# Kernel tuning notes

Hardware: AMD Instinct MI355X
Metric: run time of the kernel (lower is better)

The kernel has to match this reference:

```python
import jax, jax.numpy as jnp
import numpy as np

D = 128
N_ITERS = 3
TAU = 0.5
SCALE = D ** -0.5
NF, NV, NA = 50000, 1024, 64


def _gelu(x):
    return jax.nn.gelu(x, approximate=False)  # torch nn.GELU default = exact erf


def setup_inputs() -> dict:
    key = jax.random.key(0)
    ks = jax.random.split(key, 16)
    s = 0.02
    return {
        "fact_embs": jax.random.normal(ks[0], (NF, D), jnp.float32),
        "var_init": jax.random.normal(ks[1], (NV, D), jnp.float32),
        "cooc_mask": jax.random.randint(ks[2], (NA, NV), 0, 2, jnp.int32),
        "gumbel_u": jax.random.uniform(ks[3], (NV, NF), jnp.float32, 1e-6, 1.0 - 1e-6),
        "Wq": jax.random.normal(ks[4], (D, D), jnp.float32) * s, "bq": jnp.zeros((D,), jnp.float32),
        "Wk": jax.random.normal(ks[5], (D, D), jnp.float32) * s, "bk": jnp.zeros((D,), jnp.float32),
        "Wv": jax.random.normal(ks[6], (D, D), jnp.float32) * s, "bv": jnp.zeros((D,), jnp.float32),
        "Wm1": jax.random.normal(ks[7], (2 * D, D), jnp.float32) * s, "bm1": jnp.zeros((D,), jnp.float32),
        "Wm2": jax.random.normal(ks[8], (D, D), jnp.float32) * s, "bm2": jnp.zeros((D,), jnp.float32),
        "Wc1": jax.random.normal(ks[9], (2 * D, D), jnp.float32) * s, "bc1": jnp.zeros((D,), jnp.float32),
        "Wc2": jax.random.normal(ks[10], (D, D), jnp.float32) * s, "bc2": jnp.zeros((D,), jnp.float32),
    }


def _forward(fact_embs, var_init, gumbel_u,
             Wq, bq, Wk, bk, Wv, bv,
             Wm1, bm1, Wm2, bm2, Wc1, bc1, Wc2, bc2, cooc_mask):
    K = fact_embs @ Wk + bk          # (F, d)
    V = fact_embs @ Wv + bv          # (F, d)
    maskf = cooc_mask.astype(jnp.float32)  # (A, Nv)
    h = var_init                      # (Nv, d)

    def gate(x, W1, b1, W2, b2):
        return jax.nn.sigmoid(_gelu(x @ W1 + b1) @ W2 + b2)

    def cooc_step(h, mrow):
        # one atom's var co-occurrence update (sequential over atoms, as in torch)
        cnt = mrow.sum()
        avg = (h * mrow[:, None]).sum(0) / jnp.maximum(cnt, 1.0)  # (d,)
        avg_b = jnp.broadcast_to(avg, h.shape)
        g2 = gate(jnp.concatenate([h, avg_b], -1), Wc1, bc1, Wc2, bc2)
        upd = g2 * avg_b + (1.0 - g2) * h
        take = (cnt >= 2.0) & (mrow > 0.0)  # atoms with <2 vars skipped
        return jnp.where(take[:, None], upd, h), None

    for _ in range(N_ITERS):
        q = h @ Wq + bq                              # (Nv, d)
        scores = (q @ K.T) * SCALE                   # (Nv, F)
        attn = jax.nn.softmax(scores, axis=-1)
        ctx = attn @ V                               # (Nv, d)
        g = gate(jnp.concatenate([h, ctx], -1), Wm1, bm1, Wm2, bm2)
        h = g * ctx + (1.0 - g) * h
        h, _ = jax.lax.scan(cooc_step, h, maskf)

    # Phase 3: gumbel-softmax soft substitution + entropy regularizer
    q = h @ Wq + bq
    scores = (q @ K.T) * SCALE                       # (Nv, F)
    gumbel = -jnp.log(-jnp.log(gumbel_u))
    soft_w = jax.nn.softmax((scores + gumbel) / TAU, axis=-1)
    var_assign = soft_w @ V                          # (Nv, d) soft substitutions
    probs = jax.nn.softmax(scores, axis=-1)
    entropy = -(probs * jnp.log(probs + 1e-9)).sum()
    energy = -(soft_w * scores).sum()                # negative expected match score
    return energy, var_assign, entropy


def reference(fact_embs, var_init, cooc_mask, gumbel_u,
              Wq, bq, Wk, bk, Wv, bv,
              Wm1, bm1, Wm2, bm2, Wc1, bc1, Wc2, bc2):
    return _forward(fact_embs, var_init, gumbel_u,
                    Wq, bq, Wk, bk, Wv, bv,
                    Wm1, bm1, Wm2, bm2, Wc1, bc1, Wc2, bc2, cooc_mask)
```

## Files before the change

### kernel.cpp

```cpp
#include <hip/hip_runtime.h>
#include <hip/hip_bf16.h>
#include <math.h>

#define NF 50000
#define NFP 50048
#define NV 1024
#define NA 64
#define NSLICE 25
#define SCALE_QK 0.088388347648318447f

static const size_t OFF_KH   = 0;
static const size_t OFF_KL   = OFF_KH  + (size_t)NFP*128*2;
static const size_t OFF_VTH  = OFF_KL  + (size_t)NFP*128*2;
static const size_t OFF_VTL  = OFF_VTH + (size_t)128*NFP*2;
static const size_t OFF_P    = OFF_VTL + (size_t)128*NFP*2;
static const size_t OFF_H    = OFF_P   + (size_t)NV*NFP*2;
static const size_t OFF_QH   = OFF_H   + (size_t)NV*128*4;
static const size_t OFF_QL   = OFF_QH  + (size_t)NV*128*2;
static const size_t OFF_PART = OFF_QL  + (size_t)NV*128*2;
static const size_t OFF_ACC  = OFF_PART+ (size_t)NSLICE*NV*128*4;
static const size_t OFF_CNT  = OFF_ACC + 28672;

typedef __attribute__((ext_vector_type(8)))  short  short8;
typedef __attribute__((ext_vector_type(16))) float  floatx16;
#define MFMA32 __builtin_amdgcn_mfma_f32_32x32x16_bf16

__device__ __forceinline__ float bflo(unsigned w){ union{unsigned u;float f;}c; c.u=w<<16; return c.f; }
__device__ __forceinline__ float bfhi(unsigned w){ union{unsigned u;float f;}c; c.u=w&0xffff0000u; return c.f; }
__device__ __forceinline__ float ubf(unsigned short h){ union{unsigned u;float f;}c; c.u=((unsigned)h)<<16; return c.f; }
__device__ __forceinline__ unsigned short f2bf(float x){ __hip_bfloat16 b=__float2bfloat16(x); return *(unsigned short*)&b; }
__device__ __forceinline__ float geluf(float x){ return 0.5f*x*(1.0f+erff(x*0.70710678118654752f)); }
__device__ __forceinline__ float sigmf(float x){ return 1.0f/(1.0f+__expf(-x)); }
__device__ __forceinline__ short8 ld8(const unsigned short* p){
  union{uint4 u; short8 s;}c; c.u=*(const uint4*)p; return c.s;
}
__device__ __forceinline__ floatx16 fzero16(){
  floatx16 x;
  #pragma unroll
  for(int i=0;i<16;i++) x[i]=0.f;
  return x;
}

__device__ __forceinline__ void gridbar2(unsigned* __restrict__ barr, int bid, int t, unsigned ep){
  __syncthreads();
  if (t==0)
    __hip_atomic_store(&barr[bid<<3], ep, __ATOMIC_RELAXED, __HIP_MEMORY_SCOPE_AGENT);
  if (bid==0){
    if (t<64){
      while (__hip_atomic_load(&barr[t<<3], __ATOMIC_RELAXED, __HIP_MEMORY_SCOPE_AGENT) < ep)
        __builtin_amdgcn_s_sleep(1);
    }
    __syncthreads();
    if (t<8)
      __hip_atomic_store(&barr[512+(t<<3)], ep, __ATOMIC_RELAXED, __HIP_MEMORY_SCOPE_AGENT);
  } else if (t==0){
    while (__hip_atomic_load(&barr[512+((bid&7)<<3)], __ATOMIC_RELAXED, __HIP_MEMORY_SCOPE_AGENT) < ep)
      __builtin_amdgcn_s_sleep(1);
  }
  __syncthreads();
}

__global__ __launch_bounds__(256) void cnt_kern(const int* __restrict__ cm, float* __restrict__ cntf){
  __shared__ int sd[256];
  const int a=blockIdx.x, t=threadIdx.x;
  int s=0;
  for (int i=t;i<NV;i+=256) s+=cm[a*NV+i];
  sd[t]=s; __syncthreads();
  for (int o=128;o>0;o>>=1){ if(t<o) sd[t]+=sd[t+o]; __syncthreads(); }
  if (t==0) cntf[a]=(float)sd[0];
}

__global__ __launch_bounds__(256)
void kvproj_kern(const float* __restrict__ fe,
                 const float* __restrict__ Wk, const float* __restrict__ bk,
                 const float* __restrict__ Wv, const float* __restrict__ bv,
                 unsigned short* __restrict__ Kh, unsigned short* __restrict__ Kl,
                 unsigned short* __restrict__ Vth, unsigned short* __restrict__ Vtl){
  __shared__ float As[32][68];
  __shared__ float Bs[32][132];
  const int t=threadIdx.x;
  const int f0=blockIdx.x*64;
  const float* W  = blockIdx.y ? Wv : Wk;
  const float* bb = blockIdx.y ? bv : bk;
  float acc[4][8];
  #pragma unroll
  for(int i=0;i<4;i++){ for(int j=0;j<8;j++) acc[i][j]=0.f; }
  for (int kc=0;kc<128;kc+=32){
    { const int floc=t>>2, koff=(t&3)*8; const int f=f0+floc;
      if (f<NF){
        const float* src=fe+((size_t)f<<7)+kc+koff;
        float4 a=*(const float4*)src, b=*(const float4*)(src+4);
        As[koff+0][floc]=a.x; As[koff+1][floc]=a.y; As[koff+2][floc]=a.z; As[koff+3][floc]=a.w;
        As[koff+4][floc]=b.x; As[koff+5][floc]=b.y; As[koff+6][floc]=b.z; As[koff+7][floc]=b.w;
      } else { for(int i=0;i<8;i++) As[koff+i][floc]=0.f; } }
    { const int kk=t>>3, coff=(t&7)*16;
      const float* src=W+((size_t)(kc+kk)<<7)+coff;
      float4 a=*(const float4*)src, b=*(const float4*)(src+4), c=*(const float4*)(src+8), d=*(const float4*)(src+12);
      Bs[kk][coff+0]=a.x;Bs[kk][coff+1]=a.y;Bs[kk][coff+2]=a.z;Bs[kk][coff+3]=a.w;
      Bs[kk][coff+4]=b.x;Bs[kk][coff+5]=b.y;Bs[kk][coff+6]=b.z;Bs[kk][coff+7]=b.w;
      Bs[kk][coff+8]=c.x;Bs[kk][coff+9]=c.y;Bs[kk][coff+10]=c.z;Bs[kk][coff+11]=c.w;
      Bs[kk][coff+12]=d.x;Bs[kk][coff+13]=d.y;Bs[kk][coff+14]=d.z;Bs[kk][coff+15]=d.w; }
    __syncthreads();
    const int mloc=(t&15)*4, nloc=(t>>4)*8;
    #pragma unroll
    for (int kk=0;kk<32;kk++){
      const float4 a=*(const float4*)&As[kk][mloc];
      const float4 b0=*(const float4*)&Bs[kk][nloc];
      const float4 b1=*(const float4*)&Bs[kk][nloc+4];
      const float am[4]={a.x,a.y,a.z,a.w};
      const float bn[8]={b0.x,b0.y,b0.z,b0.w,b1.x,b1.y,b1.z,b1.w};
      #pragma unroll
      for(int mi=0;mi<4;mi++){
        #pragma unroll
        for(int ni=0;ni<8;ni++) acc[mi][ni]=fmaf(am[mi],bn[ni],acc[mi][ni]);
      }
    }
    __syncthreads();
  }
  const int mloc=(t&15)*4, nloc=(t>>4)*8;
  if (blockIdx.y==0){
    #pragma unroll
    for(int mi=0;mi<4;mi++){
      const int f=f0+mloc+mi;
      unsigned short hi[8], lo[8];
      #pragma unroll
      for(int ni=0;ni<8;ni++){
        const float o=(f<NF)? (acc[mi][ni]+bb[nloc+ni]) : 0.f;
        hi[ni]=f2bf(o); lo[ni]=f2bf(o-ubf(hi[ni]));
      }
      uint4 ph, pl;
      ph.x=(unsigned)hi[0]|((unsigned)hi[1]<<16); ph.y=(unsigned)hi[2]|((unsigned)hi[3]<<16);
      ph.z=(unsigned)hi[4]|((unsigned)hi[5]<<16); ph.w=(unsigned)hi[6]|((unsigned)hi[7]<<16);
      pl.x=(unsigned)lo[0]|((unsigned)lo[1]<<16); pl.y=(unsigned)lo[2]|((unsigned)lo[3]<<16);
      pl.z=(unsigned)lo[4]|((unsigned)lo[5]<<16); pl.w=(unsigned)lo[6]|((unsigned)lo[7]<<16);
      *(uint4*)(Kh+(size_t)f*128+nloc)=ph;
      *(uint4*)(Kl+(size_t)f*128+nloc)=pl;
    }
  } else {
    #pragma unroll
    for(int ni=0;ni<8;ni++){
      const int d=nloc+ni;
      unsigned short hi[4], lo[4];
      #pragma unroll
      for(int mi=0;mi<4;mi++){
        const int f=f0+mloc+mi;
        const float o=(f<NF)? (acc[mi][ni]+bb[d]) : 0.f;
        hi[mi]=f2bf(o); lo[mi]=f2bf(o-ubf(hi[mi]));
      }
      *(uint2*)(Vth+(size_t)d*NFP+f0+mloc)=make_uint2((unsigned)hi[0]|((unsigned)hi[1]<<16),(unsigned)hi[2]|((unsigned)hi[3]<<16));
      *(uint2*)(Vtl+(size_t)d*NFP+f0+mloc)=make_uint2((unsigned)lo[0]|((unsigned)lo[1]<<16),(unsigned)lo[2]|((unsigned)lo[3]<<16));
    }
  }
}

__global__ __launch_bounds__(128)
void qproj_kern(const float* __restrict__ h, const float* __restrict__ Wq,
                const float* __restrict__ bq,
                unsigned short* __restrict__ qh, unsigned short* __restrict__ ql){
  __shared__ float hs[128];
  const int v=blockIdx.x, c=threadIdx.x;
  hs[c]=h[(v<<7)+c];
  __syncthreads();
  float acc=bq[c];
  #pragma unroll 8
  for (int k=0;k<128;k++) acc=fmaf(hs[k],Wq[(k<<7)+c],acc);
  const unsigned short hi=f2bf(acc);
  qh[(v<<7)+c]=hi; ql[(v<<7)+c]=f2bf(acc-ubf(hi));
}

__global__ __launch_bounds__(256)
void scoresM_kern(const unsigned short* __restrict__ qh, const unsigned short* __restrict__ ql,
                  const unsigned short* __restrict__ Kh, const unsigned short* __restrict__ Kl,
                  unsigned short* __restrict__ Pb){
  const int t=threadIdx.x, w=t>>6, lane=t&63;
  const int v0=blockIdx.y*64;
  const int col=lane&31, kg=lane>>5;
  const int r0=v0+col;
  const size_t a0base=(size_t)r0*128, a1base=(size_t)(r0+32)*128;
  for (int ft=0; ft<4; ft++){
    const int fsub=blockIdx.x*512+(w+4*ft)*32;
    if (fsub>=NFP) break;
    const int f=fsub+col;
    const size_t bbase=(size_t)f*128;
    floatx16 acc0=fzero16(), acc1=fzero16();
    #pragma unroll
    for (int ks=0; ks<8; ks++){
      const int ko=ks*16+kg*8;
      short8 a0h=ld8(qh+a0base+ko), a0l=ld8(ql+a0base+ko);
      short8 a1h=ld8(qh+a1base+ko), a1l=ld8(ql+a1base+ko);
      short8 bh =ld8(Kh+bbase+ko),  bl =ld8(Kl+bbase+ko);
      acc0=MFMA32(a0h,bh,acc0,0,0,0);
      acc0=MFMA32(a0h,bl,acc0,0,0,0);
      acc0=MFMA32(a0l,bh,acc0,0,0,0);
      acc1=MFMA32(a1h,bh,acc1,0,0,0);
      acc1=MFMA32(a1h,bl,acc1,0,0,0);
      acc1=MFMA32(a1l,bh,acc1,0,0,0);
    }
    const bool inF=(f<NF);
    #pragma unroll
    for (int r=0;r<16;r++){
      const int rr=(r&3)+8*(r>>2)+4*kg;
      {
        const int row=v0+rr;
        const float s=acc0[r]*SCALE_QK;
        const float ep=inF? __expf(s):0.f;
        Pb[(size_t)row*NFP+f]=f2bf(ep);
      }
      {
        const int row=v0+32+rr;
        const float s=acc1[r]*SCALE_QK;
        const float ep=inF? __expf(s):0.f;
        Pb[(size_t)row*NFP+f]=f2bf(ep);
      }
    }
  }
}

template<int SUMZ>
__global__ __launch_bounds__(256)
void pvM_kern(const unsigned short* __restrict__ Pb,
              const unsigned short* __restrict__ Vth, const unsigned short* __restrict__ Vtl,
              float* __restrict__ part, float* __restrict__ accg){
  __shared__ float Zs[64];
  const int t=threadIdx.x, w=t>>6, lane=t&63;
  const int slice=blockIdx.x, v0=blockIdx.y*64;
  const int col=lane&31, kg=lane>>5;
  const int d0=w*32;
  const int fbeg=slice*2048, fend=min(fbeg+2048,(int)NFP);
  if (SUMZ){ if (t<64) Zs[t]=0.f; __syncthreads(); }
  floatx16 acc0=fzero16(), acc1=fzero16(), z0=fzero16(), z1=fzero16();
  const short8 ones={(short)0x3F80,(short)0x3F80,(short)0x3F80,(short)0x3F80,
                     (short)0x3F80,(short)0x3F80,(short)0x3F80,(short)0x3F80};
  const unsigned short* pr0=Pb+(size_t)(v0+col)*NFP;
  const unsigned short* pr1=Pb+(size_t)(v0+32+col)*NFP;
  const unsigned short* vh =Vth+(size_t)(d0+col)*NFP;
  const unsigned short* vl =Vtl+(size_t)(d0+col)*NFP;
  for (int fc=fbeg; fc<fend; fc+=16){
    const int ko=fc+kg*8;
    short8 a0=ld8(pr0+ko), a1=ld8(pr1+ko);
    short8 bh=ld8(vh+ko),  bl=ld8(vl+ko);
    acc0=MFMA32(a0,bh,acc0,0,0,0);
    acc0=MFMA32(a0,bl,acc0,0,0,0);
    acc1=MFMA32(a1,bh,acc1,0,0,0);
    acc1=MFMA32(a1,bl,acc1,0,0,0);
    if (SUMZ && (((fc>>4)&3)==w)){
      z0=MFMA32(a0,ones,z0,0,0,0);
      z1=MFMA32(a1,ones,z1,0,0,0);
    }
  }
  const int d=d0+col;
  #pragma unroll
  for (int r=0;r<16;r++){
    const int rr=(r&3)+8*(r>>2)+4*kg;
    part[(((size_t)slice*NV+(v0+rr))<<7)+d]   =acc0[r];
    part[(((size_t)slice*NV+(v0+32+rr))<<7)+d]=acc1[r];
  }
  if (SUMZ){
    if (col==0){
      #pragma unroll
      for (int r=0;r<16;r++){
        const int rr=(r&3)+8*(r>>2)+4*kg;
        atomicAdd(&Zs[rr],z0[r]);
        atomicAdd(&Zs[32+rr],z1[r]);
      }
    }
    __syncthreads();
    if (t<64) atomicAdd(&accg[v0+t],Zs[t]);
  }
}

__global__ __launch_bounds__(256)
void scoresF_kern(const unsigned short* __restrict__ qh, const unsigned short* __restrict__ ql,
                  const unsigned short* __restrict__ Kh, const unsigned short* __restrict__ Kl,
                  const float* __restrict__ gum, unsigned short* __restrict__ Pb,
                  float* __restrict__ accg){
  __shared__ float As[32][68];
  __shared__ float Bs[32][132];
  __shared__ float Zs[64], Zls[64], Yps[64], Yls[64];
  const int t=threadIdx.x;
  const int f0=blockIdx.x*128;
  const int v0=blockIdx.y*64;
  float acc[4][8];
  #pragma unroll
  for(int i=0;i<4;i++){ for(int j=0;j<8;j++) acc[i][j]=0.f; }
  if (t<64){ Zs[t]=0.f; Zls[t]=0.f; Yps[t]=0.f; Yls[t]=0.f; }
  for (int kc=0;kc<128;kc+=32){
    { const int vloc=t>>2, koff=(t&3)*8;
      const size_t base=((size_t)(v0+vloc)<<7)+kc+koff;
      uint4 H=*(const uint4*)(qh+base), L=*(const uint4*)(ql+base);
      As[koff+0][vloc]=bflo(H.x)+bflo(L.x); As[koff+1][vloc]=bfhi(H.x)+bfhi(L.x);
      As[koff+2][vloc]=bflo(H.y)+bflo(L.y); As[koff+3][vloc]=bfhi(H.y)+bfhi(L.y);
      As[koff+4][vloc]=bflo(H.z)+bflo(L.z); As[koff+5][vloc]=bfhi(H.z)+bfhi(L.z);
      As[koff+6][vloc]=bflo(H.w)+bflo(L.w); As[koff+7][vloc]=bfhi(H.w)+bfhi(L.w); }
    { const int floc=t>>1, koff=(t&1)*16; const int f=f0+floc;
      const size_t base=((size_t)f<<7)+kc+koff;
      uint4 H0=*(const uint4*)(Kh+base), H1=*(const uint4*)(Kh+base+8);
      uint4 L0=*(const uint4*)(Kl+base), L1=*(const uint4*)(Kl+base+8);
      Bs[koff+0][floc]=bflo(H0.x)+bflo(L0.x); Bs[koff+1][floc]=bfhi(H0.x)+bfhi(L0.x);
      Bs[koff+2][floc]=bflo(H0.y)+bflo(L0.y); Bs[koff+3][floc]=bfhi(H0.y)+bfhi(L0.y);
      Bs[koff+4][floc]=bflo(H0.z)+bflo(L0.z); Bs[koff+5][floc]=bfhi(H0.z)+bfhi(L0.z);
      Bs[koff+6][floc]=bflo(H0.w)+bflo(L0.w); Bs[koff+7][floc]=bfhi(H0.w)+bfhi(L0.w);
      Bs[koff+8][floc]=bflo(H1.x)+bflo(L1.x); Bs[koff+9][floc]=bfhi(H1.x)+bfhi(L1.x);
      Bs[koff+10][floc]=bflo(H1.y)+bflo(L1.y); Bs[koff+11][floc]=bfhi(H1.y)+bfhi(L1.y);
      Bs[koff+12][floc]=bflo(H1.z)+bflo(L1.z); Bs[koff+13][floc]=bfhi(H1.z)+bfhi(L1.z);
      Bs[koff+14][floc]=bflo(H1.w)+bflo(L1.w); Bs[koff+15][floc]=bfhi(H1.w)+bfhi(L1.w); }
    __syncthreads();
    const int mloc=(t&15)*4, nloc=(t>>4)*8;
    #pragma unroll
    for (int kk=0;kk<32;kk++){
      const float4 a=*(const float4*)&As[kk][mloc];
      const float4 b0=*(const float4*)&Bs[kk][nloc];
      const float4 b1=*(const float4*)&Bs[kk][nloc+4];
      const float am[4]={a.x,a.y,a.z,a.w};
      const float bn[8]={b0.x,b0.y,b0.z,b0.w,b1.x,b1.y,b1.z,b1.w};
      #pragma unroll
      for(int mi=0;mi<4;mi++){
        #pragma unroll
        for(int ni=0;ni<8;ni++) acc[mi][ni]=fmaf(am[mi],bn[ni],acc[mi][ni]);
      }
    }
    __syncthreads();
  }
  const int mloc=(t&15)*4, nloc=(t>>4)*8;
  #pragma unroll
  for(int mi=0;mi<4;mi++){
    const int v=v0+mloc+mi;
    float zp=0.f, zl=0.f, yp=0.f, yl=0.f;
    float uu[8];
    { const int fbase=f0+nloc;
      if (fbase+8<=NF){
        const float* gsrc=gum+(size_t)v*NF+fbase;
        float4 g0=*(const float4*)gsrc, g1=*(const float4*)(gsrc+4);
        uu[0]=g0.x;uu[1]=g0.y;uu[2]=g0.z;uu[3]=g0.w;uu[4]=g1.x;uu[5]=g1.y;uu[6]=g1.z;uu[7]=g1.w;
      } else {
        for(int i=0;i<8;i++){ int f=fbase+i; uu[i]=(f<NF)? gum[(size_t)v*NF+f] : 0.5f; }
      } }
    unsigned short pr[8];
    #pragma unroll
    for(int ni=0;ni<8;ni++){
      const int f=f0+nloc+ni;
      const float s=acc[mi][ni]*SCALE_QK;
      float pv_=0.f;
      if (f<NF){
        const float ep=__expf(s);
        const float g=-__logf(-__logf(uu[ni]));
        const float el=__expf(2.0f*(s+g));
        pv_=el; zl+=el; yl+=el*s; zp+=ep; yp+=ep*s;
      }
      pr[ni]=f2bf(pv_);
    }
    uint4 pk;
    pk.x=(unsigned)pr[0]|((unsigned)pr[1]<<16);
    pk.y=(unsigned)pr[2]|((unsigned)pr[3]<<16);
    pk.z=(unsigned)pr[4]|((unsigned)pr[5]<<16);
    pk.w=(unsigned)pr[6]|((unsigned)pr[7]<<16);
    *(uint4*)(Pb+(size_t)v*NFP+f0+nloc)=pk;
    atomicAdd(&Zs[mloc+mi],zp);
    atomicAdd(&Zls[mloc+mi],zl); atomicAdd(&Yps[mloc+mi],yp); atomicAdd(&Yls[mloc+mi],yl);
  }
  __syncthreads();
  if (t<64){
    atomicAdd(&accg[v0+t],Zs[t]);
    atomicAdd(&accg[1024+v0+t],Zls[t]);
    atomicAdd(&accg[2048+v0+t],Yps[t]);
    atomicAdd(&accg[3072+v0+t],Yls[t]);
  }
}

__global__ __launch_bounds__(256)
void gate_kern(float* __restrict__ h, const float* __restrict__ part, const float* __restrict__ Z,
               const float* __restrict__ Wm1, const float* __restrict__ bm1,
               const float* __restrict__ Wm2, const float* __restrict__ bm2){
  const int t=threadIdx.x, w=t>>6, lane=t&63;
  const int v=(blockIdx.x<<2)+w;
  const float h0=h[(v<<7)+lane], h1=h[(v<<7)+64+lane];
  const float zr=1.0f/Z[v];
  float c0=0.f,c1=0.f;
  for (int s=0;s<NSLICE;s++){
    c0+=part[(((size_t)s*NV+v)<<7)+lane];
    c1+=part[(((size_t)s*NV+v)<<7)+64+lane];
  }
  c0*=zr; c1*=zr;
  float y0=bm1[lane], y1=bm1[64+lane];
  for (int k=0;k<64;k++){ const float a=__shfl(h0,k); y0=fmaf(a,Wm1[(k<<7)+lane],y0);      y1=fmaf(a,Wm1[(k<<7)+64+lane],y1); }
  for (int k=0;k<64;k++){ const float a=__shfl(h1,k); y0=fmaf(a,Wm1[((64+k)<<7)+lane],y0); y1=fmaf(a,Wm1[((64+k)<<7)+64+lane],y1); }
  for (int k=0;k<64;k++){ const float a=__shfl(c0,k); y0=fmaf(a,Wm1[((128+k)<<7)+lane],y0);y1=fmaf(a,Wm1[((128+k)<<7)+64+lane],y1); }
  for (int k=0;k<64;k++){ const float a=__shfl(c1,k); y0=fmaf(a,Wm1[((192+k)<<7)+lane],y0);y1=fmaf(a,Wm1[((192+k)<<7)+64+lane],y1); }
  y0=geluf(y0); y1=geluf(y1);
  float z0=bm2[lane], z1=bm2[64+lane];
  for (int k=0;k<64;k++){ const float a=__shfl(y0,k); z0=fmaf(a,Wm2[(k<<7)+lane],z0);      z1=fmaf(a,Wm2[(k<<7)+64+lane],z1); }
  for (int k=0;k<64;k++){ const float a=__shfl(y1,k); z0=fmaf(a,Wm2[((64+k)<<7)+lane],z0); z1=fmaf(a,Wm2[((64+k)<<7)+64+lane],z1); }
  const float g0=sigmf(z0), g1=sigmf(z1);
  h[(v<<7)+lane]   = fmaf(g0,c0-h0,h0);
  h[(v<<7)+64+lane]= fmaf(g1,c1-h1,h1);
}

__global__ __launch_bounds__(1024,4)
void cooc_kern(float* __restrict__ h, const int* __restrict__ cm, const float* __restrict__ cntf,
               const float* __restrict__ Wc1, const float* __restrict__ bc1,
               const float* __restrict__ Wc2, const float* __restrict__ bc2,
               float* __restrict__ bufs, unsigned* __restrict__ barr){
  __shared__ float W1b[128*128];
  __shared__ unsigned short Xh[32*128], Xl[32*128];
  __shared__ unsigned short Yh[32*128], Yl[32*128];
  __shared__ float Gs[32*128];
  __shared__ float ypart2[4*128];
  __shared__ float avgs[128], seedb[128], bc1s[128], bc2s[128], cnts[64];
  __shared__ int anyf;
  const int t=threadIdx.x, w=t>>6, lane=t&63;
  const int bid=blockIdx.x;
  const int v=(bid<<4)+w;
  const int stripe=bid&7;
  const int col=lane&31, kg=lane>>5;

  for (int i=t;i<128*128;i+=1024) W1b[i]=Wc1[16384+i];
  if (t<128){ bc1s[t]=bc1[t]; bc2s[t]=bc2[t]; }
  else if (t<192) cnts[t-128]=cntf[t-128];
  for (int i=2048+t;i<4096;i+=1024){ Xh[i]=0; Xl[i]=0; }
  short8 Bh[8], Bl[8];
  {
    const float* Wsrc=(w>=4&&w<8)? Wc2 : Wc1;
    const int n0=(w&3)*32;
    #pragma unroll
    for (int ks=0;ks<8;ks++){
      #pragma unroll
      for (int j=0;j<8;j++){
        const float x=Wsrc[(ks*16+kg*8+j)*128 + n0+col];
        const unsigned short hi=f2bf(x);
        Bh[ks][j]=(short)hi; Bl[ks][j]=(short)f2bf(x-ubf(hi));
      }
    }
  }
  const unsigned long long amask=__ballot(cm[lane*NV+v]!=0);
  float h0=h[(v<<7)+lane], h1=h[(v<<7)+64+lane];
  if (t<128) seedb[t]=0.f;
  if (t==0) anyf=0;
  __syncthreads();
  if (amask&1ull){ atomicAdd(&seedb[lane],h0); atomicAdd(&seedb[64+lane],h1); if(lane==0) anyf=1; }
  __syncthreads();
  if (anyf && t<128) atomicAdd(&bufs[(stripe<<7)+t],seedb[t]);
  unsigned ep=0;
  gridbar2(barr,bid,t,++ep);

  for (int a=0;a<NA;a++){
    const int cur=a%3, nxt=(a+1)%3, zz=(a+2)%3;
    const float cf=cnts[a];
    if (w>=14){
      const int i=t-896;
      float s=0.f;
      #pragma unroll
      for (int sp=0;sp<8;sp++)
        s+=__hip_atomic_load(&bufs[(cur<<10)+(sp<<7)+i],__ATOMIC_RELAXED,__HIP_MEMORY_SCOPE_AGENT);
      avgs[i]=s/fmaxf(cf,1.0f);
    } else if (w==13){
      if (bid==0){
        #pragma unroll
        for (int sp=0;sp<8;sp++){
          __hip_atomic_store(&bufs[(zz<<10)+(sp<<7)+lane],0.0f,__ATOMIC_RELAXED,__HIP_MEMORY_SCOPE_AGENT);
          __hip_atomic_store(&bufs[(zz<<10)+(sp<<7)+64+lane],0.0f,__ATOMIC_RELAXED,__HIP_MEMORY_SCOPE_AGENT);
        }
      }
    } else if (w==12){
      seedb[lane]=0.f; seedb[64+lane]=0.f;
      if (lane==0) anyf=0;
    }
    {
      const unsigned short h0h=f2bf(h0), h1h=f2bf(h1);
      const unsigned short h0l=f2bf(h0-ubf(h0h)), h1l=f2bf(h1-ubf(h1h));
      const int sw=(w&7)<<3;
      Xh[(w<<7)+(lane^sw)]=h0h;      Xl[(w<<7)+(lane^sw)]=h0l;
      Xh[(w<<7)+((64+lane)^sw)]=h1h; Xl[(w<<7)+((64+lane)^sw)]=h1l;
    }
    __syncthreads();
    floatx16 accY=fzero16();
    if (w<4){
      #pragma unroll
      for (int ks=0;ks<8;ks++){
        const int ko=ks*16+kg*8;
        const int ridx=(col<<7)+(ko^((col&7)<<3));
        short8 ah=ld8(&Xh[ridx]), al=ld8(&Xl[ridx]);
        accY=MFMA32(ah,Bh[ks],accY,0,0,0);
        accY=MFMA32(al,Bh[ks],accY,0,0,0);
        accY=MFMA32(ah,Bl[ks],accY,0,0,0);
      }
    } else if (w>=8){
      const int idx=t-512, ss=idx>>7, c2=idx&127;
      float acc=0.f;
      #pragma unroll
      for (int j=0;j<32;j++) acc=fmaf(avgs[ss*32+j],W1b[(ss*32+j)*128+c2],acc);
      ypart2[ss*128+c2]=acc;
    }
    __syncthreads();
    if (w<4){
      const int c=(w<<5)+col;
      const float yav=ypart2[c]+ypart2[128+c]+ypart2[256+c]+ypart2[384+c]+bc1s[c];
      #pragma unroll
      for (int r=0;r<16;r++){
        const int rr=(r&3)+8*(r>>2)+4*kg;
        const float yv=geluf(accY[r]+yav);
        const unsigned short yh=f2bf(yv);
        const unsigned short yl=f2bf(yv-ubf(yh));
        const int wi=(rr<<7)+(c^((rr&7)<<3));
        Yh[wi]=yh; Yl[wi]=yl;
      }
    }
    __syncthreads();
    if (w>=4&&w<8){
      floatx16 accZ=fzero16();
      #pragma unroll
      for (int ks=0;ks<8;ks++){
        const int ko=ks*16+kg*8;
        const int ridx=(col<<7)+(ko^((col&7)<<3));
        short8 ah=ld8(&Yh[ridx]), al=ld8(&Yl[ridx]);
        accZ=MFMA32(ah,Bh[ks],accZ,0,0,0);
        accZ=MFMA32(al,Bh[ks],accZ,0,0,0);
        accZ=MFMA32(ah,Bl[ks],accZ,0,0,0);
      }
      const int c=((w-4)<<5)+col;
      const float b2=bc2s[c];
      #pragma unroll
      for (int r=0;r<16;r++){
        const int rr=(r&3)+8*(r>>2)+4*kg;
        Gs[(rr<<7)+c]=sigmf(accZ[r]+b2);
      }
    }
    __syncthreads();
    {
      const bool act=((amask>>a)&1ull)&&(cf>=2.0f);
      if (act){
        const float g0=Gs[(w<<7)+lane], g1=Gs[(w<<7)+64+lane];
        h0=fmaf(g0,avgs[lane]-h0,h0);
        h1=fmaf(g1,avgs[64+lane]-h1,h1);
      }
    }
    if (a<NA-1){
      if ((amask>>(a+1))&1ull){
        atomicAdd(&seedb[lane],h0); atomicAdd(&seedb[64+lane],h1);
        if (lane==0) anyf=1;
      }
      __syncthreads();
      if (anyf && t<128)
        atomicAdd(&bufs[(nxt<<10)+(stripe<<7)+t],seedb[t]);
      gridbar2(barr,bid,t,++ep);
    }
  }
  h[(v<<7)+lane]=h0; h[(v<<7)+64+lane]=h1;
}

__global__ __launch_bounds__(256)
void writeout_kern(const float* __restrict__ accg, const float* __restrict__ part,
                   float* __restrict__ out){
  const int b=blockIdx.x, t=threadIdx.x;
  const int v0=b*16;
  for (int i=t;i<16*128;i+=256){
    const int v=v0+(i>>7), d=i&127;
    float s=0.f;
    for (int sl=0;sl<NSLICE;sl++) s+=part[(((size_t)sl*NV+v)<<7)+d];
    out[1+((size_t)v<<7)+d]=s/accg[1024+v];
  }
  __shared__ float es[16], hsv[16];
  if (t<16){
    const int v=v0+t;
    const float Zp=accg[v], Zl=accg[1024+v], Yp=accg[2048+v], Yl=accg[3072+v];
    es[t]=-Yl/Zl;
    hsv[t]=-(Yp/Zp-logf(Zp));
  }
  __syncthreads();
  if (t==0){
    float a=0.f,c=0.f;
    for(int i=0;i<16;i++){ a+=es[i]; c+=hsv[i]; }
    atomicAdd(&out[0],a);
    atomicAdd(&out[1+(size_t)NV*128],c);
  }
}

extern "C" void kernel_launch(void* const* d_in, const int* in_sizes, int n_in,
                              void* d_out, int out_size, void* d_ws, size_t ws_size,
                              hipStream_t stream){
  (void)in_sizes; (void)n_in; (void)ws_size;
  const float* fe =(const float*)d_in[0];
  const float* vi =(const float*)d_in[1];
  const int*   cm =(const int*)  d_in[2];
  const float* gum=(const float*)d_in[3];
  const float* Wq =(const float*)d_in[4];  const float* bq =(const float*)d_in[5];
  const float* Wk =(const float*)d_in[6];  const float* bk =(const float*)d_in[7];
  const float* Wv =(const float*)d_in[8];  const float* bv =(const float*)d_in[9];
  const float* Wm1=(const float*)d_in[10]; const float* bm1=(const float*)d_in[11];
  const float* Wm2=(const float*)d_in[12]; const float* bm2=(const float*)d_in[13];
  const float* Wc1=(const float*)d_in[14]; const float* bc1=(const float*)d_in[15];
  const float* Wc2=(const float*)d_in[16]; const float* bc2=(const float*)d_in[17];
  float* out=(float*)d_out;
  char* w8=(char*)d_ws;
  unsigned short* Kh =(unsigned short*)(w8+OFF_KH);
  unsigned short* Kl =(unsigned short*)(w8+OFF_KL);
  unsigned short* Vth=(unsigned short*)(w8+OFF_VTH);
  unsigned short* Vtl=(unsigned short*)(w8+OFF_VTL);
  unsigned short* Pb =(unsigned short*)(w8+OFF_P);
  float* hb  =(float*)(w8+OFF_H);
  unsigned short* qhb=(unsigned short*)(w8+OFF_QH);
  unsigned short* qlb=(unsigned short*)(w8+OFF_QL);
  float* part=(float*)(w8+OFF_PART);
  float* accb=(float*)(w8+OFF_ACC);
  float* avgb=accb+4096;
  float* cntf=(float*)(w8+OFF_CNT);
  unsigned* barr=(unsigned*)(w8+OFF_P);

  hipMemsetAsync(out,0,(size_t)out_size*4,stream);
  hipMemcpyAsync(hb,vi,(size_t)NV*128*4,hipMemcpyDeviceToDevice,stream);
  cnt_kern<<<NA,256,0,stream>>>(cm,cntf);
  kvproj_kern<<<dim3(NFP/64,2),256,0,stream>>>(fe,Wk,bk,Wv,bv,Kh,Kl,Vth,Vtl);

  for (int it=0; it<3; it++){
    hipMemsetAsync(accb,0,28672,stream);
    qproj_kern<<<NV,128,0,stream>>>(hb,Wq,bq,qhb,qlb);
    scoresM_kern<<<dim3(98,16),256,0,stream>>>(qhb,qlb,Kh,Kl,Pb);
    pvM_kern<1><<<dim3(NSLICE,16),256,0,stream>>>(Pb,Vth,Vtl,part,accb);
    gate_kern<<<NV/4,256,0,stream>>>(hb,part,accb,Wm1,bm1,Wm2,bm2);
    hipMemsetAsync(barr,0,2304,stream);
    cooc_kern<<<64,1024,0,stream>>>(hb,cm,cntf,Wc1,bc1,Wc2,bc2,avgb,barr);
  }

  hipMemsetAsync(accb,0,28672,stream);
  qproj_kern<<<NV,128,0,stream>>>(hb,Wq,bq,qhb,qlb);
  scoresF_kern<<<dim3(NFP/128,16),256,0,stream>>>(qhb,qlb,Kh,Kl,gum,Pb,accb);
  pvM_kern<0><<<dim3(NSLICE,16),256,0,stream>>>(Pb,Vth,Vtl,part,accb);
  writeout_kern<<<64,256,0,stream>>>(accb,part,out);
}
```

Before: 4.346 ms.

## Shrink cooc kernel to 8 blocks with flag-based slot exchange instead of grid barrier

The sequential co-occurrence scan now runs on 8 workgroups of 1024 threads, each owning 128 variable rows, instead of 64 workgroups of 16 rows. The two-level grid barrier and the atomically accumulated striped buffers are replaced by per-block partial-sum slots and monotonically increasing per-block flags that each block polls. The aim is to cut the cost of synchronising 64 times per iteration across many blocks. In exchange, each block does more MFMA and register work per atom (both weight matrices are held in registers, plus 8 rows per wave) on fewer CUs.

```diff
diff --git a/kernel.cpp b/kernel.cpp
--- a/kernel.cpp
+++ b/kernel.cpp
@@ -39,25 +39,6 @@
   #pragma unroll
   for(int i=0;i<16;i++) x[i]=0.f;
   return x;
-}
-
-__device__ __forceinline__ void gridbar2(unsigned* __restrict__ barr, int bid, int t, unsigned ep){
-  __syncthreads();
-  if (t==0)
-    __hip_atomic_store(&barr[bid<<3], ep, __ATOMIC_RELAXED, __HIP_MEMORY_SCOPE_AGENT);
-  if (bid==0){
-    if (t<64){
-      while (__hip_atomic_load(&barr[t<<3], __ATOMIC_RELAXED, __HIP_MEMORY_SCOPE_AGENT) < ep)
-        __builtin_amdgcn_s_sleep(1);
-    }
-    __syncthreads();
-    if (t<8)
-      __hip_atomic_store(&barr[512+(t<<3)], ep, __ATOMIC_RELAXED, __HIP_MEMORY_SCOPE_AGENT);
-  } else if (t==0){
-    while (__hip_atomic_load(&barr[512+((bid&7)<<3)], __ATOMIC_RELAXED, __HIP_MEMORY_SCOPE_AGENT) < ep)
-      __builtin_amdgcn_s_sleep(1);
-  }
-  __syncthreads();
 }
 
 __global__ __launch_bounds__(256) void cnt_kern(const int* __restrict__ cm, float* __restrict__ cntf){
@@ -395,156 +376,165 @@
   h[(v<<7)+64+lane]= fmaf(g1,c1-h1,h1);
 }
 
-__global__ __launch_bounds__(1024,4)
+__global__ __launch_bounds__(1024,1)
 void cooc_kern(float* __restrict__ h, const int* __restrict__ cm, const float* __restrict__ cntf,
                const float* __restrict__ Wc1, const float* __restrict__ bc1,
                const float* __restrict__ Wc2, const float* __restrict__ bc2,
-               float* __restrict__ bufs, unsigned* __restrict__ barr){
-  __shared__ float W1b[128*128];
-  __shared__ unsigned short Xh[32*128], Xl[32*128];
-  __shared__ unsigned short Yh[32*128], Yl[32*128];
-  __shared__ float Gs[32*128];
-  __shared__ float ypart2[4*128];
+               float* __restrict__ slots, unsigned* __restrict__ flags){
+  __shared__ unsigned short XBUF[2*128*128];
+  __shared__ unsigned short Yh[128*128], Yl[128*128];
+  __shared__ float ypart2[8*128];
   __shared__ float avgs[128], seedb[128], bc1s[128], bc2s[128], cnts[64];
-  __shared__ int anyf;
+  unsigned short* Xh=XBUF;
+  unsigned short* Xl=XBUF+16384;
+  float* Gs=(float*)XBUF;
   const int t=threadIdx.x, w=t>>6, lane=t&63;
   const int bid=blockIdx.x;
-  const int v=(bid<<4)+w;
-  const int stripe=bid&7;
   const int col=lane&31, kg=lane>>5;
-
-  for (int i=t;i<128*128;i+=1024) W1b[i]=Wc1[16384+i];
-  if (t<128){ bc1s[t]=bc1[t]; bc2s[t]=bc2[t]; }
+  const int rt=w&3, ct=w>>2, n0=ct*32;
+  const int v0=(bid<<7)+(w<<3);
+
+  if (t<128){ bc1s[t]=bc1[t]; bc2s[t]=bc2[t]; seedb[t]=0.f; }
   else if (t<192) cnts[t-128]=cntf[t-128];
-  for (int i=2048+t;i<4096;i+=1024){ Xh[i]=0; Xl[i]=0; }
-  short8 Bh[8], Bl[8];
-  {
-    const float* Wsrc=(w>=4&&w<8)? Wc2 : Wc1;
-    const int n0=(w&3)*32;
-    #pragma unroll
-    for (int ks=0;ks<8;ks++){
-      #pragma unroll
-      for (int j=0;j<8;j++){
-        const float x=Wsrc[(ks*16+kg*8+j)*128 + n0+col];
-        const unsigned short hi=f2bf(x);
-        Bh[ks][j]=(short)hi; Bl[ks][j]=(short)f2bf(x-ubf(hi));
-      }
-    }
-  }
-  const unsigned long long amask=__ballot(cm[lane*NV+v]!=0);
-  float h0=h[(v<<7)+lane], h1=h[(v<<7)+64+lane];
-  if (t<128) seedb[t]=0.f;
-  if (t==0) anyf=0;
+  short8 B1h[8],B1l[8],B2h[8],B2l[8];
+  #pragma unroll
+  for (int ks=0;ks<8;ks++){
+    #pragma unroll
+    for (int j=0;j<8;j++){
+      const int k=ks*16+kg*8+j;
+      const float x1=Wc1[k*128+n0+col];
+      const float x2=Wc2[k*128+n0+col];
+      const unsigned short h1v=f2bf(x1), h2v=f2bf(x2);
+      B1h[ks][j]=(short)h1v; B1l[ks][j]=(short)f2bf(x1-ubf(h1v));
+      B2h[ks][j]=(short)h2v; B2l[ks][j]=(short)f2bf(x2-ubf(h2v));
+    }
+  }
+  unsigned long long amask[8];
+  float h0[8], h1[8];
+  #pragma unroll
+  for (int j=0;j<8;j++){
+    amask[j]=__ballot(cm[lane*NV+(v0+j)]!=0);
+    h0[j]=h[((v0+j)<<7)+lane];
+    h1[j]=h[((v0+j)<<7)+64+lane];
+  }
   __syncthreads();
-  if (amask&1ull){ atomicAdd(&seedb[lane],h0); atomicAdd(&seedb[64+lane],h1); if(lane==0) anyf=1; }
+  { float s0=0.f,s1=0.f;
+    #pragma unroll
+    for (int j=0;j<8;j++) if (amask[j]&1ull){ s0+=h0[j]; s1+=h1[j]; }
+    atomicAdd(&seedb[lane],s0); atomicAdd(&seedb[64+lane],s1); }
   __syncthreads();
-  if (anyf && t<128) atomicAdd(&bufs[(stripe<<7)+t],seedb[t]);
-  unsigned ep=0;
-  gridbar2(barr,bid,t,++ep);
+  if (t<128){ float s=seedb[t]; seedb[t]=0.f;
+    __hip_atomic_store(&slots[(bid<<7)+t], s, __ATOMIC_RELAXED, __HIP_MEMORY_SCOPE_AGENT); }
+  __syncthreads();
+  if (t==0) __hip_atomic_store(&flags[bid<<5], 1u, __ATOMIC_RELAXED, __HIP_MEMORY_SCOPE_AGENT);
 
   for (int a=0;a<NA;a++){
-    const int cur=a%3, nxt=(a+1)%3, zz=(a+2)%3;
     const float cf=cnts[a];
-    if (w>=14){
-      const int i=t-896;
+    #pragma unroll
+    for (int j=0;j<8;j++){
+      const int row=(w<<3)+j;
+      const int sw=(row&15)<<3;
+      const unsigned short h0h=f2bf(h0[j]), h1h=f2bf(h1[j]);
+      const unsigned short h0l=f2bf(h0[j]-ubf(h0h)), h1l=f2bf(h1[j]-ubf(h1h));
+      Xh[(row<<7)+(lane^sw)]=h0h;      Xl[(row<<7)+(lane^sw)]=h0l;
+      Xh[(row<<7)+((64+lane)^sw)]=h1h; Xl[(row<<7)+((64+lane)^sw)]=h1l;
+    }
+    __syncthreads();
+    if (t<8){
+      while (__hip_atomic_load(&flags[t<<5], __ATOMIC_RELAXED, __HIP_MEMORY_SCOPE_AGENT) < (unsigned)(a+1))
+        __builtin_amdgcn_s_sleep(1);
+    }
+    __syncthreads();
+    if (t<128){
       float s=0.f;
+      const int e=(a%3)<<10;
       #pragma unroll
       for (int sp=0;sp<8;sp++)
-        s+=__hip_atomic_load(&bufs[(cur<<10)+(sp<<7)+i],__ATOMIC_RELAXED,__HIP_MEMORY_SCOPE_AGENT);
-      avgs[i]=s/fmaxf(cf,1.0f);
-    } else if (w==13){
-      if (bid==0){
-        #pragma unroll
-        for (int sp=0;sp<8;sp++){
-          __hip_atomic_store(&bufs[(zz<<10)+(sp<<7)+lane],0.0f,__ATOMIC_RELAXED,__HIP_MEMORY_SCOPE_AGENT);
-          __hip_atomic_store(&bufs[(zz<<10)+(sp<<7)+64+lane],0.0f,__ATOMIC_RELAXED,__HIP_MEMORY_SCOPE_AGENT);
-        }
-      }
-    } else if (w==12){
-      seedb[lane]=0.f; seedb[64+lane]=0.f;
-      if (lane==0) anyf=0;
-    }
-    {
-      const unsigned short h0h=f2bf(h0), h1h=f2bf(h1);
-      const unsigned short h0l=f2bf(h0-ubf(h0h)), h1l=f2bf(h1-ubf(h1h));
-      const int sw=(w&7)<<3;
-      Xh[(w<<7)+(lane^sw)]=h0h;      Xl[(w<<7)+(lane^sw)]=h0l;
-      Xh[(w<<7)+((64+lane)^sw)]=h1h; Xl[(w<<7)+((64+lane)^sw)]=h1l;
-    }
-    __syncthreads();
+        s+=__hip_atomic_load(&slots[e+(sp<<7)+t], __ATOMIC_RELAXED, __HIP_MEMORY_SCOPE_AGENT);
+      avgs[t]=s/fmaxf(cf,1.0f);
+    }
+    __syncthreads();
+    { const int seg=t>>7, c2=t&127, kb=seg<<4;
+      float sacc=0.f;
+      #pragma unroll
+      for (int j=0;j<16;j++) sacc=fmaf(avgs[kb+j],Wc1[(128+kb+j)*128+c2],sacc);
+      ypart2[(seg<<7)+c2]=sacc; }
     floatx16 accY=fzero16();
-    if (w<4){
+    { const int arow=(rt<<5)+col;
+      const int sw=(arow&15)<<3;
       #pragma unroll
       for (int ks=0;ks<8;ks++){
-        const int ko=ks*16+kg*8;
-        const int ridx=(col<<7)+(ko^((col&7)<<3));
-        short8 ah=ld8(&Xh[ridx]), al=ld8(&Xl[ridx]);
-        accY=MFMA32(ah,Bh[ks],accY,0,0,0);
-        accY=MFMA32(al,Bh[ks],accY,0,0,0);
-        accY=MFMA32(ah,Bl[ks],accY,0,0,0);
-      }
-    } else if (w>=8){
-      const int idx=t-512, ss=idx>>7, c2=idx&127;
-      float acc=0.f;
-      #pragma unroll
-      for (int j=0;j<32;j++) acc=fmaf(avgs[ss*32+j],W1b[(ss*32+j)*128+c2],acc);
-      ypart2[ss*128+c2]=acc;
-    }
-    __syncthreads();
-    if (w<4){
-      const int c=(w<<5)+col;
-      const float yav=ypart2[c]+ypart2[128+c]+ypart2[256+c]+ypart2[384+c]+bc1s[c];
+        const int ko=(ks*16+kg*8)^sw;
+        short8 ah=ld8(&Xh[(arow<<7)+ko]), al=ld8(&Xl[(arow<<7)+ko]);
+        accY=MFMA32(ah,B1h[ks],accY,0,0,0);
+        accY=MFMA32(al,B1h[ks],accY,0,0,0);
+        accY=MFMA32(ah,B1l[ks],accY,0,0,0);
+      } }
+    __syncthreads();
+    { const int c=n0+col;
+      float yav=bc1s[c];
+      #pragma unroll
+      for (int seg=0;seg<8;seg++) yav+=ypart2[(seg<<7)+c];
       #pragma unroll
       for (int r=0;r<16;r++){
         const int rr=(r&3)+8*(r>>2)+4*kg;
+        const int row=(rt<<5)+rr;
         const float yv=geluf(accY[r]+yav);
         const unsigned short yh=f2bf(yv);
         const unsigned short yl=f2bf(yv-ubf(yh));
-        const int wi=(rr<<7)+(c^((rr&7)<<3));
+        const int wi=(row<<7)+(c^((row&15)<<3));
         Yh[wi]=yh; Yl[wi]=yl;
-      }
-    }
-    __syncthreads();
-    if (w>=4&&w<8){
-      floatx16 accZ=fzero16();
+      } }
+    __syncthreads();
+    { floatx16 accZ=fzero16();
+      const int arow=(rt<<5)+col;
+      const int sw=(arow&15)<<3;
       #pragma unroll
       for (int ks=0;ks<8;ks++){
-        const int ko=ks*16+kg*8;
-        const int ridx=(col<<7)+(ko^((col&7)<<3));
-        short8 ah=ld8(&Yh[ridx]), al=ld8(&Yl[ridx]);
-        accZ=MFMA32(ah,Bh[ks],accZ,0,0,0);
-        accZ=MFMA32(al,Bh[ks],accZ,0,0,0);
-        accZ=MFMA32(ah,Bl[ks],accZ,0,0,0);
-      }
-      const int c=((w-4)<<5)+col;
+        const int ko=(ks*16+kg*8)^sw;
+        short8 ah=ld8(&Yh[(arow<<7)+ko]), al=ld8(&Yl[(arow<<7)+ko]);
+        accZ=MFMA32(ah,B2h[ks],accZ,0,0,0);
+        accZ=MFMA32(al,B2h[ks],accZ,0,0,0);
+        accZ=MFMA32(ah,B2l[ks],accZ,0,0,0);
+      }
+      const int c=n0+col;
       const float b2=bc2s[c];
       #pragma unroll
       for (int r=0;r<16;r++){
         const int rr=(r&3)+8*(r>>2)+4*kg;
-        Gs[(rr<<7)+c]=sigmf(accZ[r]+b2);
-      }
-    }
-    __syncthreads();
-    {
-      const bool act=((amask>>a)&1ull)&&(cf>=2.0f);
-      if (act){
-        const float g0=Gs[(w<<7)+lane], g1=Gs[(w<<7)+64+lane];
-        h0=fmaf(g0,avgs[lane]-h0,h0);
-        h1=fmaf(g1,avgs[64+lane]-h1,h1);
-      }
-    }
+        const int row=(rt<<5)+rr;
+        Gs[(row<<7)+c]=sigmf(accZ[r]+b2);
+      } }
+    __syncthreads();
+    { const float av0=avgs[lane], av1=avgs[64+lane];
+      const bool cok=(cf>=2.0f);
+      float s0=0.f,s1=0.f;
+      #pragma unroll
+      for (int j=0;j<8;j++){
+        const int row=(w<<3)+j;
+        if (cok && ((amask[j]>>a)&1ull)){
+          const float g0=Gs[(row<<7)+lane], g1=Gs[(row<<7)+64+lane];
+          h0[j]=fmaf(g0,av0-h0[j],h0[j]);
+          h1[j]=fmaf(g1,av1-h1[j],h1[j]);
+        }
+        if (a<NA-1 && ((amask[j]>>(a+1))&1ull)){ s0+=h0[j]; s1+=h1[j]; }
+      }
+      if (a<NA-1){ atomicAdd(&seedb[lane],s0); atomicAdd(&seedb[64+lane],s1); } }
+    __syncthreads();
     if (a<NA-1){
-      if ((amask>>(a+1))&1ull){
-        atomicAdd(&seedb[lane],h0); atomicAdd(&seedb[64+lane],h1);
-        if (lane==0) anyf=1;
+      if (t<128){
+        const float s=seedb[t]; seedb[t]=0.f;
+        __hip_atomic_store(&slots[(((a+1)%3)<<10)+(bid<<7)+t], s, __ATOMIC_RELAXED, __HIP_MEMORY_SCOPE_AGENT);
       }
       __syncthreads();
-      if (anyf && t<128)
-        atomicAdd(&bufs[(nxt<<10)+(stripe<<7)+t],seedb[t]);
-      gridbar2(barr,bid,t,++ep);
-    }
-  }
-  h[(v<<7)+lane]=h0; h[(v<<7)+64+lane]=h1;
+      if (t==0) __hip_atomic_store(&flags[bid<<5], (unsigned)(a+2), __ATOMIC_RELAXED, __HIP_MEMORY_SCOPE_AGENT);
+    }
+  }
+  #pragma unroll
+  for (int j=0;j<8;j++){
+    h[((v0+j)<<7)+lane]   =h0[j];
+    h[((v0+j)<<7)+64+lane]=h1[j];
+  }
 }
 
 __global__ __launch_bounds__(256)
@@ -601,9 +591,9 @@
   unsigned short* qlb=(unsigned short*)(w8+OFF_QL);
   float* part=(float*)(w8+OFF_PART);
   float* accb=(float*)(w8+OFF_ACC);
-  float* avgb=accb+4096;
+  float* slots=accb+4096;
   float* cntf=(float*)(w8+OFF_CNT);
-  unsigned* barr=(unsigned*)(w8+OFF_P);
+  unsigned* flags=(unsigned*)(w8+OFF_P);
 
   hipMemsetAsync(out,0,(size_t)out_size*4,stream);
   hipMemcpyAsync(hb,vi,(size_t)NV*128*4,hipMemcpyDeviceToDevice,stream);
@@ -616,8 +606,8 @@
     scoresM_kern<<<dim3(98,16),256,0,stream>>>(qhb,qlb,Kh,Kl,Pb);
     pvM_kern<1><<<dim3(NSLICE,16),256,0,stream>>>(Pb,Vth,Vtl,part,accb);
     gate_kern<<<NV/4,256,0,stream>>>(hb,part,accb,Wm1,bm1,Wm2,bm2);
-    hipMemsetAsync(barr,0,2304,stream);
-    cooc_kern<<<64,1024,0,stream>>>(hb,cm,cntf,Wc1,bc1,Wc2,bc2,avgb,barr);
+    hipMemsetAsync(flags,0,2304,stream);
+    cooc_kern<<<8,1024,0,stream>>>(hb,cm,cntf,Wc1,bc1,Wc2,bc2,slots,flags);
   }
 
   hipMemsetAsync(accb,0,28672,stream);
```

After: 6.249 ms. +43.8%, slower.
